# Performance work log

Hardware: AMD Instinct MI355X
Metric: run time of the kernel (lower is better)

## Reference

```python
import jax, jax.numpy as jnp
import numpy as np

B, C, H, W = 16, 1536, 32, 32
M = 64      # num_clusters
L = 128     # cluster_dim
G = 256     # token_dim
HID = 512
OT_ITERS = 3
EPS = 1e-6


def setup_inputs() -> dict:
    key = jax.random.key(0)
    ks = jax.random.split(key, 12)
    def w(k, shape, fan_in):
        return jax.random.normal(k, shape, jnp.float32) * (1.0 / np.sqrt(fan_in))
    return {
        'x': jax.random.normal(ks[0], (B, C, H, W), jnp.float32),
        't': jax.random.normal(ks[1], (B, C), jnp.float32),
        # token_features: Linear(C->512), ReLU, Linear(512->G)
        'Wt1': w(ks[2], (HID, C), C), 'bt1': jnp.zeros((HID,), jnp.float32),
        'Wt2': w(ks[3], (G, HID), HID), 'bt2': jnp.zeros((G,), jnp.float32),
        # cluster_features: 1x1 Conv(C->512), ReLU, 1x1 Conv(512->L)
        'Wc1': w(ks[4], (HID, C), C), 'bc1': jnp.zeros((HID,), jnp.float32),
        'Wc2': w(ks[5], (L, HID), HID), 'bc2': jnp.zeros((L,), jnp.float32),
        # score: 1x1 Conv(C->512), ReLU, 1x1 Conv(512->M)
        'Ws1': w(ks[6], (HID, C), C), 'bs1': jnp.zeros((HID,), jnp.float32),
        'Ws2': w(ks[7], (M, HID), HID), 'bs2': jnp.zeros((M,), jnp.float32),
        # temp_predictor: Conv1d(L->1, k=1)
        'Wtp': w(ks[8], (L,), L), 'btp': jnp.zeros((), jnp.float32),
        'dust_bin': jnp.asarray(1.0, jnp.float32),
        'burst_b': jnp.asarray(0.0, jnp.float32),
        'burst_p': jnp.asarray(1.0, jnp.float32),
        'lambda_discount': jnp.asarray(0.5, jnp.float32),
    }


def _log_optimal_transport(scores, alpha, iters):
    # scores: [B, m, n]; alpha: scalar dust-bin logit
    b, m, n = scores.shape
    Z0 = jnp.concatenate([scores, jnp.broadcast_to(alpha, (b, 1, n))], axis=1)  # [B, m+1, n]
    norm = -jnp.log(jnp.asarray(m + n, scores.dtype))
    log_mu = jnp.concatenate([jnp.full((m,), norm, scores.dtype),
                              (jnp.log(jnp.asarray(n, scores.dtype)) + norm)[None]])  # [m+1]
    log_nu = jnp.full((n,), norm, scores.dtype)
    u = jnp.zeros((b, m + 1), scores.dtype)
    v = jnp.zeros((b, n), scores.dtype)
    for _ in range(iters):
        u = log_mu - jax.nn.logsumexp(Z0 + v[:, None, :], axis=2)
        v = log_nu - jax.nn.logsumexp(Z0 + u[:, :, None], axis=1)
    return Z0 + u[:, :, None] + v[:, None, :] - norm


def _l2norm(a, axis):
    return a / jnp.maximum(jnp.linalg.norm(a, axis=axis, keepdims=True), 1e-12)


def _forward(x, t, Wt1, bt1, Wt2, bt2, Wc1, bc1, Wc2, bc2, Ws1, bs1, Ws2, bs2,
             Wtp, btp, dust_bin, burst_b, burst_p, lambda_discount):
    b, c, h, w = x.shape
    n = h * w
    xf = x.reshape(b, c, n)  # [B, C, N] (1x1 convs == per-pixel MLP)
    # cluster features f: [B, L, N]
    h1 = jax.nn.relu(jnp.einsum('bcn,oc->bon', xf, Wc1) + bc1[:, None])
    f = jnp.einsum('bhn,lh->bln', h1, Wc2) + bc2[:, None]
    # assignment scores p: [B, M, N]
    h2 = jax.nn.relu(jnp.einsum('bcn,oc->bon', xf, Ws1) + bs1[:, None])
    p = jnp.einsum('bhn,mh->bmn', h2, Ws2) + bs2[:, None]
    # global token: [B, G]
    tok = jax.nn.relu(t @ Wt1.T + bt1) @ Wt2.T + bt2
    # Sinkhorn OT soft assignment, drop dust bin row
    P = jnp.exp(_log_optimal_transport(p, dust_bin, OT_ITERS))[:, :-1, :]  # [B, M, N]
    # burst-aware weighting
    f_norm = _l2norm(f, axis=1)                                  # [B, L, N]
    T_i = jax.nn.softplus(jnp.einsum('bln,l->bn', f, Wtp) + btp)  # [B, N]
    sim = jnp.einsum('bli,blj->bij', f_norm, f_norm)              # [B, N, N]
    T_avg = (T_i[:, :, None] + T_i[:, None, :]) * 0.5
    burst_w = jax.nn.sigmoid(T_avg * sim + burst_b)
    discount = jnp.clip(jnp.sum(burst_w, axis=-1) ** burst_p, 1e-3, 1e3)  # [B, N]
    lam = jax.nn.sigmoid(lambda_discount)
    P_adj = (1.0 - lam) * P + lam * (P / (discount[:, None, :] + EPS))
    # local aggregation: (f[:, :, None, :] * P[:, None, :, :]).sum(-1) == batched matmul
    agg = jnp.einsum('bln,bmn->blm', f, P_adj)  # [B, L, M]
    agg = _l2norm(agg, axis=1).reshape(b, -1)   # [B, L*M]
    tok_n = _l2norm(tok, axis=-1)
    g = jnp.concatenate([tok_n, agg], axis=-1)  # [B, G + L*M]
    return _l2norm(g, axis=-1)


def reference(x, t, Wt1, bt1, Wt2, bt2, Wc1, bc1, Wc2, bc2, Ws1, bs1, Ws2, bs2,
              Wtp, btp, dust_bin, burst_b, burst_p, lambda_discount):
    return _forward(x, t, Wt1, bt1, Wt2, bt2, Wc1, bc1, Wc2, bc2, Ws1, bs1, Ws2, bs2,
                    Wtp, btp, dust_bin, burst_b, burst_p, lambda_discount)
```

## Files before the change

kernel.cpp:

```cpp
#include <hip/hip_runtime.h>
#include <math.h>

#define B_   16
#define C_   1536
#define N_   1024
#define M_   64
#define L_   128
#define G_   256
#define HID_ 512

typedef __attribute__((ext_vector_type(8))) short short8;
typedef __attribute__((ext_vector_type(4))) float floatx4;

__device__ __forceinline__ unsigned short f2bf_rne(float x) {
    unsigned u = __float_as_uint(x);
    unsigned r = u + 0x7fffu + ((u >> 16) & 1u);
    return (unsigned short)(r >> 16);
}
__device__ __forceinline__ unsigned pack_bf2(float lo, float hi) {
    unsigned a = __float_as_uint(lo) + 0x8000u;
    unsigned b = __float_as_uint(hi) + 0x8000u;
    return (a >> 16) | (b & 0xffff0000u);
}

__device__ __forceinline__ void gl2lds16(const void* g, void* l) {
    __builtin_amdgcn_global_load_lds(
        (const __attribute__((address_space(1))) void*)g,
        (__attribute__((address_space(3))) void*)l, 16, 0, 0);
}

__global__ __launch_bounds__(256) void cast_w_kernel(
    const float* __restrict__ Wc1, const float* __restrict__ Ws1,
    const float* __restrict__ Wc2, const float* __restrict__ Ws2,
    unsigned short* __restrict__ Wbf, unsigned short* __restrict__ W2)
{
    const int V1 = 393216;
    const int VH = 196608;
    int idx = blockIdx.x * 256 + threadIdx.x;
    if (idx < V1) {
        const float4* src = (idx < VH) ? (const float4*)Wc1 : (const float4*)Ws1;
        float4 v = src[(idx < VH) ? idx : idx - VH];
        ushort4 o;
        o.x = f2bf_rne(v.x); o.y = f2bf_rne(v.y);
        o.z = f2bf_rne(v.z); o.w = f2bf_rne(v.w);
        ((ushort4*)Wbf)[idx] = o;
    } else if (idx < V1 + 192 * 1024) {
        int i2 = idx - V1;
        int row = i2 >> 10, k = i2 & 1023;
        float v = 0.f;
        if (row < 128) { if (k < 512) v = Wc2[row * 512 + k]; }
        else           { if (k >= 512) v = Ws2[(row - 128) * 512 + (k - 512)]; }
        W2[i2] = f2bf_rne(v);
    }
}

__global__ __launch_bounds__(256) void xt_kernel(
    const float* __restrict__ x, unsigned short* __restrict__ xT)
{
    __shared__ float Xs[64][65];
    const int t = threadIdx.x;
    const int n0 = blockIdx.x * 64, c0 = blockIdx.y * 64, b = blockIdx.z;
    const float* xb = x + (long)b * C_ * N_;
    #pragma unroll
    for (int it = 0; it < 16; ++it) {
        int idx = it * 256 + t, cr = idx >> 6, nc = idx & 63;
        Xs[cr][nc] = xb[(long)(c0 + cr) * N_ + n0 + nc];
    }
    __syncthreads();
    unsigned* xo = (unsigned*)(xT + (long)b * N_ * C_);
    #pragma unroll
    for (int it = 0; it < 8; ++it) {
        int idx = it * 256 + t, nr = idx >> 5, pc = idx & 31;
        xo[(long)(n0 + nr) * 768 + (c0 >> 1) + pc] =
            pack_bf2(Xs[2 * pc][nr], Xs[2 * pc + 1][nr]);
    }
}

#define G1_STAGE_A(kt, q)                                                    \
    gl2lds16(aSrc + (long)(q) * (32 * C_) + (kt) * 64,                       \
             (char*)g1lds + (((kt) & 1) * 65536 + (q) * 8192) + sdst)
#define G1_STAGE_B(kt, q)                                                    \
    gl2lds16(bSrc + (long)(q) * (32 * C_) + (kt) * 64,                       \
             (char*)g1lds + (((kt) & 1) * 65536 + 32768 + (q) * 8192) + sdst)

#define G1_PHASE(q, STAGES, TAIL)                                            \
  {                                                                          \
    const char* ab = cb + aFB + (q) * 8192;                                  \
    short8 a0 = *(const short8*)(ab + ks0);                                  \
    short8 a1 = *(const short8*)(ab + ks1);                                  \
    short8 a2 = *(const short8*)(ab + 2048 + ks0);                           \
    short8 a3 = *(const short8*)(ab + 2048 + ks1);                           \
    STAGES                                                                   \
    __builtin_amdgcn_s_barrier();                                            \
    asm volatile("s_waitcnt lgkmcnt(0)" ::: "memory");                       \
    __builtin_amdgcn_sched_barrier(0);                                       \
    __builtin_amdgcn_s_setprio(1);                                           \
    _Pragma("unroll")                                                        \
    for (int fj = 0; fj < 4; ++fj) {                                         \
      acc[2*(q)][fj]   = __builtin_amdgcn_mfma_f32_16x16x32_bf16(            \
          a0, bfr[fj][0], acc[2*(q)][fj], 0, 0, 0);                          \
      acc[2*(q)][fj]   = __builtin_amdgcn_mfma_f32_16x16x32_bf16(            \
          a1, bfr[fj][1], acc[2*(q)][fj], 0, 0, 0);                          \
      acc[2*(q)+1][fj] = __builtin_amdgcn_mfma_f32_16x16x32_bf16(            \
          a2, bfr[fj][0], acc[2*(q)+1][fj], 0, 0, 0);                        \
      acc[2*(q)+1][fj] = __builtin_amdgcn_mfma_f32_16x16x32_bf16(            \
          a3, bfr[fj][1], acc[2*(q)+1][fj], 0, 0, 0);                        \
    }                                                                        \
    __builtin_amdgcn_s_setprio(0);                                           \
    TAIL                                                                     \
    __builtin_amdgcn_s_barrier();                                            \
    __builtin_amdgcn_sched_barrier(0);                                       \
  }

#define G1_TILE(tt, S1, S2, TAIL3)                                           \
  {                                                                          \
    const char* cb = (const char*)g1lds + ((tt) & 1) * 65536;                \
    _Pragma("unroll")                                                        \
    for (int fj = 0; fj < 4; ++fj) {                                         \
      const char* bb = cb + bFB + (fj >> 1) * 8192 + (fj & 1) * 2048;        \
      bfr[fj][0] = *(const short8*)(bb + ks0);                               \
      bfr[fj][1] = *(const short8*)(bb + ks1);                               \
    }                                                                        \
    G1_PHASE(0, if (S1) { G1_STAGE_A((tt)+1, 2); G1_STAGE_A((tt)+1, 3); }, ) \
    G1_PHASE(1, if (S2) { G1_STAGE_B((tt)+2, 0); G1_STAGE_B((tt)+2, 1); }, ) \
    G1_PHASE(2, if (S2) { G1_STAGE_B((tt)+2, 2); G1_STAGE_B((tt)+2, 3); }, ) \
    G1_PHASE(3, if (S2) { G1_STAGE_A((tt)+2, 0); G1_STAGE_A((tt)+2, 1); }, TAIL3) \
  }

__global__ __launch_bounds__(512, 2) void gemm1_kernel(
    const unsigned short* __restrict__ Wbf, const unsigned short* __restrict__ xT,
    const float* __restrict__ bc1, const float* __restrict__ bs1,
    unsigned short* __restrict__ hT)
{
    __shared__ unsigned short g1lds[65536];
    const int t = threadIdx.x;
    const int lane = t & 63, w = t >> 6;
    const int n0 = blockIdx.x * 256, o0 = blockIdx.y * 256, b = blockIdx.z;

    const int sgrow = ((t & 256) ? 128 : 0) + ((t >> 3) & 31);
    const int sdst  = t * 16;
    const int sslot = ((t & 7) ^ ((t >> 3) & 7)) * 8;
    const unsigned short* aSrc = Wbf + (long)(o0 + sgrow) * C_ + sslot;
    const unsigned short* bSrc = xT + (long)b * N_ * C_
                               + (long)(n0 + sgrow) * C_ + sslot;

    const int lrow = lane & 15, kgrp = lane >> 4;
    const int wo = (w >> 2) * 128, wn = (w & 3) * 64;
    const int aFB = (w >> 2) * 4096 + lrow * 128;
    const int bFB = 32768 + ((w >> 1) & 1) * 4096 + (w & 1) * 16384 + lrow * 128;
    const int ks0 = (kgrp ^ (lrow & 7)) * 16;
    const int ks1 = ((4 + kgrp) ^ (lrow & 7)) * 16;

    floatx4 acc[8][4];
    #pragma unroll
    for (int i = 0; i < 8; ++i)
        #pragma unroll
        for (int j = 0; j < 4; ++j) acc[i][j] = (floatx4)0.0f;
    short8 bfr[4][2];

    #pragma unroll
    for (int q = 0; q < 4; ++q) { G1_STAGE_A(0, q); G1_STAGE_B(0, q); }
    #pragma unroll
    for (int q = 0; q < 4; ++q) G1_STAGE_B(1, q);
    G1_STAGE_A(1, 0); G1_STAGE_A(1, 1);
    asm volatile("s_waitcnt vmcnt(6)" ::: "memory");
    __builtin_amdgcn_s_barrier();
    __builtin_amdgcn_sched_barrier(0);

    #pragma unroll 2
    for (int t8 = 0; t8 < 22; ++t8)
        G1_TILE(t8, 1, 1, asm volatile("s_waitcnt vmcnt(6)" ::: "memory");)
    G1_TILE(22, 1, 0, asm volatile("s_waitcnt vmcnt(0)" ::: "memory");)
    G1_TILE(23, 0, 0, )

    const float* bias = (o0 < 512) ? bc1 : bs1;
    const int ob = (o0 < 512) ? o0 : o0 - 512;
    #pragma unroll
    for (int fi = 0; fi < 8; ++fi) {
        const int orow = wo + fi * 16 + kgrp * 4;
        float4 bv = *(const float4*)&bias[ob + orow];
        #pragma unroll
        for (int fj = 0; fj < 4; ++fj) {
            const int n = n0 + wn + fj * 16 + lrow;
            float v0 = fmaxf(acc[fi][fj][0] + bv.x, 0.f);
            float v1 = fmaxf(acc[fi][fj][1] + bv.y, 0.f);
            float v2 = fmaxf(acc[fi][fj][2] + bv.z, 0.f);
            float v3 = fmaxf(acc[fi][fj][3] + bv.w, 0.f);
            uint2 pk;
            pk.x = ((unsigned)f2bf_rne(v0)) | (((unsigned)f2bf_rne(v1)) << 16);
            pk.y = ((unsigned)f2bf_rne(v2)) | (((unsigned)f2bf_rne(v3)) << 16);
            *(uint2*)&hT[((long)b * N_ + n) * 1024 + o0 + orow] = pk;
        }
    }
}

__global__ __launch_bounds__(256, 2) void gemm23_kernel(
    const unsigned short* __restrict__ W2, const unsigned short* __restrict__ hT,
    const float* __restrict__ bc2, const float* __restrict__ bs2,
    float* __restrict__ f, float* __restrict__ p)
{
    __shared__ unsigned short As[64 * 32];
    __shared__ unsigned short Bs[128 * 32];
    const int t = threadIdx.x;
    const int lane = t & 63, w = t >> 6;
    const int n0 = blockIdx.x * 128, o0 = blockIdx.y * 64, b = blockIdx.z;
    const unsigned short* hTb = hT + (long)b * N_ * 1024;

    const int wo = (w >> 1) * 32, wn = (w & 1) * 64;
    const int lrow = lane & 15, kgrp = lane >> 4;
    const int arow = t >> 2, acol = (t & 3) * 8;
    const int klo = (o0 < 128) ? 0 : 512;

    floatx4 acc[2][4];
    #pragma unroll
    for (int i = 0; i < 2; ++i)
        #pragma unroll
        for (int j = 0; j < 4; ++j) acc[i][j] = (floatx4)0.0f;

    for (int k0 = 0; k0 < 512; k0 += 32) {
        gl2lds16(W2 + (long)(o0 + arow) * 1024 + klo + k0 + acol, (char*)As + t * 16);
        #pragma unroll
        for (int r = 0; r < 2; ++r)
            gl2lds16(hTb + (long)(n0 + r * 64 + arow) * 1024 + klo + k0 + acol,
                     (char*)Bs + r * 4096 + t * 16);
        __syncthreads();
        short8 af[2], bfr[4];
        #pragma unroll
        for (int i = 0; i < 2; ++i)
            af[i] = *(const short8*)((const char*)As +
                        (wo + i * 16 + lrow) * 64 + kgrp * 16);
        #pragma unroll
        for (int j = 0; j < 4; ++j)
            bfr[j] = *(const short8*)((const char*)Bs +
                        (wn + j * 16 + lrow) * 64 + kgrp * 16);
        #pragma unroll
        for (int i = 0; i < 2; ++i)
            #pragma unroll
            for (int j = 0; j < 4; ++j)
                acc[i][j] = __builtin_amdgcn_mfma_f32_16x16x32_bf16(
                    af[i], bfr[j], acc[i][j], 0, 0, 0);
        __syncthreads();
    }

    #pragma unroll
    for (int i = 0; i < 2; ++i) {
        int o = o0 + wo + i * 16 + kgrp * 4;
        #pragma unroll
        for (int j = 0; j < 4; ++j) {
            int n = n0 + wn + j * 16 + lrow;
            #pragma unroll
            for (int r = 0; r < 4; ++r) {
                int oo = o + r;
                float v = acc[i][j][r];
                if (oo < 128) f[((long)b * L_ + oo) * N_ + n] = v + bc2[oo];
                else p[((long)b * M_ + (oo - 128)) * N_ + n] = v + bs2[oo - 128];
            }
        }
    }
}

__global__ __launch_bounds__(256) void token1_kernel(
    const float* __restrict__ t_in, const float* __restrict__ Wt1,
    const float* __restrict__ bt1, float* __restrict__ hid)
{
    const int lane = threadIdx.x & 63, w = threadIdx.x >> 6;
    const int o = blockIdx.x * 4 + w, b = blockIdx.y;
    const float4* wr = (const float4*)(Wt1 + (long)o * C_);
    const float4* tb = (const float4*)(t_in + (long)b * C_);
    float acc = 0.f;
    #pragma unroll
    for (int i = 0; i < 6; ++i) {
        float4 a = wr[i * 64 + lane], tv = tb[i * 64 + lane];
        acc += a.x * tv.x + a.y * tv.y + a.z * tv.z + a.w * tv.w;
    }
    #pragma unroll
    for (int off = 1; off < 64; off <<= 1) acc += __shfl_xor(acc, off);
    if (lane == 0) hid[b * HID_ + o] = fmaxf(acc + bt1[o], 0.f);
}

__global__ __launch_bounds__(256) void token2_kernel(
    const float* __restrict__ hid, const float* __restrict__ Wt2,
    const float* __restrict__ bt2, float* __restrict__ tok)
{
    const int lane = threadIdx.x & 63, w = threadIdx.x >> 6;
    const int g = blockIdx.x * 4 + w, b = blockIdx.y;
    const float4* wr = (const float4*)(Wt2 + (long)g * HID_);
    const float4* hb = (const float4*)(hid + (long)b * HID_);
    float acc = 0.f;
    #pragma unroll
    for (int i = 0; i < 2; ++i) {
        float4 a = wr[i * 64 + lane], hv = hb[i * 64 + lane];
        acc += a.x * hv.x + a.y * hv.y + a.z * hv.z + a.w * hv.w;
    }
    #pragma unroll
    for (int off = 1; off < 64; off <<= 1) acc += __shfl_xor(acc, off);
    if (lane == 0) tok[b * G_ + g] = acc + bt2[g];
}

__global__ __launch_bounds__(256) void token3_kernel(
    const float* __restrict__ tok, float* __restrict__ tokn)
{
    __shared__ float red[4];
    const int b = blockIdx.x, t = threadIdx.x;
    float v = tok[b * G_ + t];
    float ss = v * v;
    #pragma unroll
    for (int off = 1; off < 64; off <<= 1) ss += __shfl_xor(ss, off);
    if ((t & 63) == 0) red[t >> 6] = ss;
    __syncthreads();
    float inv = 1.f / fmaxf(sqrtf(red[0] + red[1] + red[2] + red[3]), 1e-12f);
    tokn[b * G_ + t] = v * inv;
}

template<bool FIRST>
__global__ __launch_bounds__(256) void ku_kernel(
    float* __restrict__ p, const float* __restrict__ dust,
    const float* __restrict__ bvec, float* __restrict__ avec)
{
    const int t = threadIdx.x, lane = t & 63, w = t >> 6;
    const int m = blockIdx.x * 4 + w, b = blockIdx.y;
    if (m > M_) return;
    const float* bv = bvec + b * N_;
    float s = 0.f;
    if (m < M_) {
        float* row = p + ((long)b * M_ + m) * N_;
        #pragma unroll
        for (int i = 0; i < 16; ++i) {
            int n = i * 64 + lane;
            if (FIRST) {
                float K = expf(row[n]);
                row[n] = K;
                s += K;
            } else {
                s += row[n] * bv[n];
            }
        }
    } else {
        float ea = expf(dust[0]);
        if (FIRST) s = 16.f * ea;
        else {
            #pragma unroll
            for (int i = 0; i < 16; ++i) s += bv[i * 64 + lane];
            s *= ea;
        }
    }
    #pragma unroll
    for (int off = 1; off < 64; off <<= 1) s += __shfl_xor(s, off);
    if (lane == 0) {
        float mu = (m < M_) ? (1.f / 1088.f) : (1024.f / 1088.f);
        avec[b * (M_ + 1) + m] = mu / s;
    }
}

__global__ __launch_bounds__(256) void kv_kernel(
    const float* __restrict__ K, const float* __restrict__ dust,
    const float* __restrict__ avec, float* __restrict__ bvec)
{
    __shared__ float a_s[M_ + 1];
    const int t = threadIdx.x, b = blockIdx.y;
    const int n = blockIdx.x * 256 + t;
    if (t < M_ + 1) a_s[t] = avec[b * (M_ + 1) + t];
    __syncthreads();
    float s = expf(dust[0]) * a_s[M_];
    const float* col = K + (long)b * M_ * N_ + n;
    #pragma unroll
    for (int m = 0; m < M_; ++m) s = fmaf(col[(long)m * N_], a_s[m], s);
    bvec[b * N_ + n] = (1.f / 1088.f) / s;
}

__global__ __launch_bounds__(256) void tnorm_kernel(
    const float* __restrict__ f, const float* __restrict__ Wtp,
    const float* __restrict__ btp, unsigned short* __restrict__ fnT,
    float* __restrict__ T, float* __restrict__ draw, float* __restrict__ aggz)
{
    __shared__ float Ft[L_][65];
    __shared__ float red_ss[4][64];
    __shared__ float red_dot[4][64];
    __shared__ float invs[64];
    __shared__ float wtp_s[L_];
    const int b = blockIdx.y, n0 = blockIdx.x * 64, t = threadIdx.x;
    const float* fb = f + (long)b * L_ * N_;

    if (t < L_) wtp_s[t] = Wtp[t];
    for (int it = 0; it < 32; ++it) {
        int idx = it * 256 + t;
        int l = idx >> 6, c = idx & 63;
        Ft[l][c] = fb[(long)l * N_ + n0 + c];
    }
    __syncthreads();
    {
        const int lg = t >> 6, col = t & 63;
        float ss = 0.f, dot = 0.f;
        #pragma unroll
        for (int i = 0; i < 32; ++i) {
            int l = lg * 32 + i;
            float v = Ft[l][col];
            ss = fmaf(v, v, ss);
            dot = fmaf(v, wtp_s[l], dot);
        }
        red_ss[lg][col] = ss;
        red_dot[lg][col] = dot;
    }
    {
        int base = (b * 16 + blockIdx.x) * 512;
        aggz[base + t] = 0.f;
        aggz[base + 256 + t] = 0.f;
    }
    __syncthreads();
    if (t < 64) {
        float ss = ((red_ss[0][t] + red_ss[1][t]) + (red_ss[2][t] + red_ss[3][t]));
        float dot = ((red_dot[0][t] + red_dot[1][t]) + (red_dot[2][t] + red_dot[3][t]));
        invs[t] = 1.f / fmaxf(sqrtf(ss), 1e-12f);
        float xx = dot + btp[0];
        T[b * N_ + n0 + t] = (xx > 0.f) ? (xx + log1pf(expf(-xx)))
                                        : log1pf(expf(xx));
        draw[b * N_ + n0 + t] = 0.f;
    }
    __syncthreads();
    unsigned* fo = (unsigned*)fnT;
    for (int it = 0; it < 16; ++it) {
        int idx = it * 256 + t;
        int nl = idx >> 6, jp = idx & 63;
        float inv = invs[nl];
        fo[(((long)b * N_ + n0 + nl) << 6) + jp] =
            pack_bf2(Ft[2 * jp][nl] * inv, Ft[2 * jp + 1][nl] * inv);
    }
}

__global__ __launch_bounds__(256) void sim_kernel(
    const unsigned short* __restrict__ fnT, const float* __restrict__ T,
    const float* __restrict__ bb, float* __restrict__ draw)
{
    __shared__ unsigned short As[64 * 136];
    __shared__ unsigned short Bs[64 * 136];
    __shared__ float Ti[64], Tj[64];
    const int b = blockIdx.z, i0 = blockIdx.y * 64, j0base = blockIdx.x * 256;
    const int t = threadIdx.x, lane = t & 63, w = t >> 6;
    const int lrow = lane & 15, kgrp = lane >> 4;
    const unsigned short* fb = fnT + (long)b * N_ * 128;
    const float burstb = bb[0];

    if (t < 64) Ti[t] = T[b * N_ + i0 + t];
    const int srow = t >> 4, scol = (t & 15) * 8;
    #pragma unroll
    for (int r = 0; r < 4; ++r) {
        uint4 av = *(const uint4*)(fb + (long)(i0 + r * 16 + srow) * 128 + scol);
        *(uint4*)((char*)As + (r * 16 + srow) * 272 + scol * 2) = av;
    }
    uint4 bv[4];
    #pragma unroll
    for (int r = 0; r < 4; ++r)
        bv[r] = *(const uint4*)(fb + (long)(j0base + r * 16 + srow) * 128 + scol);

    float rs[4] = {0.f, 0.f, 0.f, 0.f};
    #pragma unroll
    for (int jj = 0; jj < 4; ++jj) {
        __syncthreads();
        #pragma unroll
        for (int r = 0; r < 4; ++r)
            *(uint4*)((char*)Bs + (r * 16 + srow) * 272 + scol * 2) = bv[r];
        if (t >= 64 && t < 128) Tj[t - 64] = T[b * N_ + j0base + jj * 64 + (t - 64)];
        if (jj < 3) {
            #pragma unroll
            for (int r = 0; r < 4; ++r)
                bv[r] = *(const uint4*)(fb +
                    (long)(j0base + (jj + 1) * 64 + r * 16 + srow) * 128 + scol);
        }
        __syncthreads();

        floatx4 acc[4];
        #pragma unroll
        for (int j = 0; j < 4; ++j) acc[j] = (floatx4)0.0f;
        __builtin_amdgcn_s_setprio(1);
        #pragma unroll
        for (int k0 = 0; k0 < 128; k0 += 32) {
            short8 af = *(const short8*)((const char*)As +
                            (w * 16 + lrow) * 272 + k0 * 2 + kgrp * 16);
            #pragma unroll
            for (int j = 0; j < 4; ++j) {
                short8 bf = *(const short8*)((const char*)Bs +
                                (j * 16 + lrow) * 272 + k0 * 2 + kgrp * 16);
                acc[j] = __builtin_amdgcn_mfma_f32_16x16x32_bf16(af, bf, acc[j], 0, 0, 0);
            }
        }
        __builtin_amdgcn_s_setprio(0);
        #pragma unroll
        for (int j = 0; j < 4; ++j) {
            float Tjv = Tj[j * 16 + lrow];
            #pragma unroll
            for (int r = 0; r < 4; ++r) {
                float Tiv = Ti[w * 16 + kgrp * 4 + r];
                float xarg = 0.5f * (Tiv + Tjv) * acc[j][r] + burstb;
                rs[r] += 1.f / (1.f + expf(-xarg));
            }
        }
    }

    #pragma unroll
    for (int off = 1; off < 16; off <<= 1)
        #pragma unroll
        for (int r = 0; r < 4; ++r) rs[r] += __shfl_xor(rs[r], off);
    if (lrow == 0) {
        #pragma unroll
        for (int r = 0; r < 4; ++r)
            atomicAdd(&draw[b * N_ + i0 + w * 16 + kgrp * 4 + r], rs[r]);
    }
}

__global__ __launch_bounds__(256) void agg_kernel(
    const float* __restrict__ f, const float* __restrict__ Kmat,
    const float* __restrict__ avec, const float* __restrict__ dust,
    const float* __restrict__ draw, const float* __restrict__ bp,
    const float* __restrict__ lamd, float* __restrict__ agg)
{
    __shared__ float fch[L_][65];
    __shared__ float Pch[M_][65];
    __shared__ float a_s[M_ + 1], cf[64];
    const int b = blockIdx.y, n0 = blockIdx.x * 64;
    const int t = threadIdx.x, tx = t & 15, ty = t >> 4;
    const float* fb = f + (long)b * L_ * N_;
    const float* Kb = Kmat + (long)b * M_ * N_;

    if (t < M_ + 1) a_s[t] = avec[b * (M_ + 1) + t];
    __syncthreads();

    for (int idx = t; idx < L_ * 64; idx += 256) {
        int l = idx >> 6, c = idx & 63;
        fch[l][c] = fb[(long)l * N_ + n0 + c];
    }
    for (int idx = t; idx < M_ * 64; idx += 256) {
        int m = idx >> 6, c = idx & 63;
        Pch[m][c] = Kb[(long)m * N_ + n0 + c] * a_s[m];
    }
    __syncthreads();

    if (t < 64) {
        float s = expf(dust[0]) * a_s[M_];
        #pragma unroll
        for (int m = 0; m < M_; ++m) s += Pch[m][t];
        float d = powf(draw[b * N_ + n0 + t], bp[0]);
        d = fminf(fmaxf(d, 1e-3f), 1e3f);
        float lam = 1.f / (1.f + expf(-lamd[0]));
        cf[t] = ((1.f - lam) + lam / (d + 1e-6f)) / s;
    }
    __syncthreads();

    float acc[8][4] = {};
    for (int n = 0; n < 64; ++n) {
        float cfn = cf[n];
        float fv[8], pv[4];
        #pragma unroll
        for (int i = 0; i < 8; ++i) fv[i] = fch[ty + 16 * i][n];
        #pragma unroll
        for (int j = 0; j < 4; ++j) pv[j] = Pch[tx * 4 + j][n] * cfn;
        #pragma unroll
        for (int i = 0; i < 8; ++i)
            #pragma unroll
            for (int j = 0; j < 4; ++j)
                acc[i][j] = fmaf(fv[i], pv[j], acc[i][j]);
    }
    #pragma unroll
    for (int i = 0; i < 8; ++i)
        #pragma unroll
        for (int j = 0; j < 4; ++j)
            atomicAdd(&agg[((long)b * L_ + (ty + 16 * i)) * M_ + tx * 4 + j],
                      acc[i][j]);
}

__global__ __launch_bounds__(256) void final_kernel(
    const float* __restrict__ tokn, const float* __restrict__ agg,
    float* __restrict__ out)
{
    __shared__ float invm[M_];
    __shared__ float red[4];
    __shared__ float s_invtot;
    const int b = blockIdx.x, t = threadIdx.x;
    const float* ab = agg + (long)b * L_ * M_;

    if (t < 64) {
        float ss = 0.f;
        for (int l = 0; l < L_; ++l) {
            float v = ab[l * M_ + t];
            ss = fmaf(v, v, ss);
        }
        invm[t] = 1.f / fmaxf(sqrtf(ss), 1e-12f);
    }
    __syncthreads();

    float part;
    {
        float tn = tokn[b * G_ + t];
        part = tn * tn;
    }
    for (int idx = t; idx < L_ * M_; idx += 256) {
        float v = ab[idx] * invm[idx & 63];
        part = fmaf(v, v, part);
    }
    for (int off = 32; off; off >>= 1) part += __shfl_down(part, off);
    if ((t & 63) == 0) red[t >> 6] = part;
    __syncthreads();
    if (t == 0)
        s_invtot = 1.f / fmaxf(sqrtf(red[0] + red[1] + red[2] + red[3]), 1e-12f);
    __syncthreads();

    const float invtot = s_invtot;
    float* ob = out + (long)b * (G_ + L_ * M_);
    ob[t] = tokn[b * G_ + t] * invtot;
    for (int idx = t; idx < L_ * M_; idx += 256)
        ob[G_ + idx] = ab[idx] * invm[idx & 63] * invtot;
}

extern "C" void kernel_launch(void* const* d_in, const int* in_sizes, int n_in,
                              void* d_out, int out_size, void* d_ws, size_t ws_size,
                              hipStream_t stream)
{
    const float* x    = (const float*)d_in[0];
    const float* t_in = (const float*)d_in[1];
    const float* Wt1  = (const float*)d_in[2];
    const float* bt1  = (const float*)d_in[3];
    const float* Wt2  = (const float*)d_in[4];
    const float* bt2  = (const float*)d_in[5];
    const float* Wc1  = (const float*)d_in[6];
    const float* bc1  = (const float*)d_in[7];
    const float* Wc2  = (const float*)d_in[8];
    const float* bc2  = (const float*)d_in[9];
    const float* Ws1  = (const float*)d_in[10];
    const float* bs1  = (const float*)d_in[11];
    const float* Ws2  = (const float*)d_in[12];
    const float* bs2  = (const float*)d_in[13];
    const float* Wtp  = (const float*)d_in[14];
    const float* btp  = (const float*)d_in[15];
    const float* dust = (const float*)d_in[16];
    const float* bb   = (const float*)d_in[17];
    const float* bp   = (const float*)d_in[18];
    const float* lamd = (const float*)d_in[19];

    char* wsb = (char*)d_ws;
    unsigned short* xT  = (unsigned short*)wsb;
    float* f    = (float*)(wsb + 0);
    float* p    = (float*)(wsb + 8388608);
    unsigned short* fnT = (unsigned short*)(wsb + 12582912);
    float* hid  = (float*)(wsb + 16777216);
    float* tok  = (float*)(wsb + 16809984);
    float* tokn = (float*)(wsb + 16826368);
    float* T    = (float*)(wsb + 16842752);
    float* draw = (float*)(wsb + 16908288);
    float* agg  = (float*)(wsb + 17039360);
    float* avec = (float*)(wsb + 17563648);
    float* bvec = (float*)(wsb + 17567808);
    unsigned short* hT  = (unsigned short*)(wsb + 50331648);
    unsigned short* Wbf = (unsigned short*)(wsb + 83886080);
    unsigned short* W2  = (unsigned short*)(wsb + 87031808);
    float* out  = (float*)d_out;

    cast_w_kernel<<<2304, 256, 0, stream>>>(Wc1, Ws1, Wc2, Ws2, Wbf, W2);

    xt_kernel   <<<dim3(16, 24, 16), 256, 0, stream>>>(x, xT);
    gemm1_kernel<<<dim3(4, 4, 16), 512, 0, stream>>>(Wbf, xT, bc1, bs1, hT);
    gemm23_kernel<<<dim3(8, 3, 16), 256, 0, stream>>>(W2, hT, bc2, bs2, f, p);

    token1_kernel<<<dim3(128, 16), 256, 0, stream>>>(t_in, Wt1, bt1, hid);
    token2_kernel<<<dim3(64, 16), 256, 0, stream>>>(hid, Wt2, bt2, tok);
    token3_kernel<<<16, 256, 0, stream>>>(tok, tokn);

    ku_kernel<true> <<<dim3(17, 16), 256, 0, stream>>>(p, dust, bvec, avec);
    kv_kernel       <<<dim3(4, 16), 256, 0, stream>>>(p, dust, avec, bvec);
    ku_kernel<false><<<dim3(17, 16), 256, 0, stream>>>(p, dust, bvec, avec);
    kv_kernel       <<<dim3(4, 16), 256, 0, stream>>>(p, dust, avec, bvec);
    ku_kernel<false><<<dim3(17, 16), 256, 0, stream>>>(p, dust, bvec, avec);

    tnorm_kernel<<<dim3(16, 16), 256, 0, stream>>>(f, Wtp, btp, fnT, T, draw, agg);
    sim_kernel  <<<dim3(4, 16, 16), 256, 0, stream>>>(fnT, T, bb, draw);
    agg_kernel  <<<dim3(16, 16), 256, 0, stream>>>(f, p, avec, dust, draw, bp, lamd, agg);
    final_kernel<<<16, 256, 0, stream>>>(tokn, agg, out);
}
```

Measured before the change: 384.1 us.

## Fuse Sinkhorn iterations into one persistent kernel with per-batch grid barriers

Replaces the five separate row/column normalization launches with one persistent kernel of 256 blocks. Each block keeps its four exp'd score rows in LDS, accumulates column sums through atomics, and synchronizes the 16 blocks of each batch with a global-atomic spin barrier. The exp is recomputed in agg_kernel instead of writing K back to memory. This removes launch overhead and repeated global reads of the score matrix. In exchange it relies on all 256 blocks being co-resident for the barrier to avoid deadlock, and the atomic float sums are nondeterministic.

```diff
diff --git a/kernel.cpp b/kernel.cpp
--- a/kernel.cpp
+++ b/kernel.cpp
@@ -29,13 +29,26 @@
         (__attribute__((address_space(3))) void*)l, 16, 0, 0);
 }
 
+__device__ __forceinline__ void bar16(unsigned* c, int gen) {
+    __threadfence();
+    __syncthreads();
+    if (threadIdx.x == 0) {
+        __hip_atomic_fetch_add(&c[gen], 1u, __ATOMIC_ACQ_REL, __HIP_MEMORY_SCOPE_AGENT);
+        while (__hip_atomic_load(&c[gen], __ATOMIC_ACQUIRE, __HIP_MEMORY_SCOPE_AGENT) < 16u)
+            __builtin_amdgcn_s_sleep(1);
+    }
+    __syncthreads();
+}
+
 __global__ __launch_bounds__(256) void cast_w_kernel(
     const float* __restrict__ Wc1, const float* __restrict__ Ws1,
     const float* __restrict__ Wc2, const float* __restrict__ Ws2,
-    unsigned short* __restrict__ Wbf, unsigned short* __restrict__ W2)
+    unsigned short* __restrict__ Wbf, unsigned short* __restrict__ W2,
+    float* __restrict__ colsum, unsigned* __restrict__ ctr)
 {
     const int V1 = 393216;
     const int VH = 196608;
+    const int E2 = V1 + 192 * 1024;
     int idx = blockIdx.x * 256 + threadIdx.x;
     if (idx < V1) {
         const float4* src = (idx < VH) ? (const float4*)Wc1 : (const float4*)Ws1;
@@ -44,13 +57,17 @@
         o.x = f2bf_rne(v.x); o.y = f2bf_rne(v.y);
         o.z = f2bf_rne(v.z); o.w = f2bf_rne(v.w);
         ((ushort4*)Wbf)[idx] = o;
-    } else if (idx < V1 + 192 * 1024) {
+    } else if (idx < E2) {
         int i2 = idx - V1;
         int row = i2 >> 10, k = i2 & 1023;
         float v = 0.f;
         if (row < 128) { if (k < 512) v = Wc2[row * 512 + k]; }
         else           { if (k >= 512) v = Ws2[(row - 128) * 512 + (k - 512)]; }
         W2[i2] = f2bf_rne(v);
+    } else if (idx < E2 + 32768) {
+        colsum[idx - E2] = 0.f;
+    } else if (idx < E2 + 32768 + 128) {
+        ctr[idx - E2 - 32768] = 0u;
     }
 }
 
@@ -312,60 +329,116 @@
     tokn[b * G_ + t] = v * inv;
 }
 
-template<bool FIRST>
-__global__ __launch_bounds__(256) void ku_kernel(
-    float* __restrict__ p, const float* __restrict__ dust,
-    const float* __restrict__ bvec, float* __restrict__ avec)
-{
+#define SK_C1 (1.f/1088.f)
+__global__ __launch_bounds__(256) void sinkhorn_persist(
+    const float* __restrict__ p, const float* __restrict__ dust,
+    float* __restrict__ avec, float* __restrict__ colsum,
+    unsigned* __restrict__ ctr)
+{
+    __shared__ float Klds[4][1024];
+    __shared__ float b_lds[1024];
+    __shared__ float a4[4];
+    __shared__ float red[4];
+    const int s = blockIdx.x, b = blockIdx.y;
     const int t = threadIdx.x, lane = t & 63, w = t >> 6;
-    const int m = blockIdx.x * 4 + w, b = blockIdx.y;
-    if (m > M_) return;
-    const float* bv = bvec + b * N_;
-    float s = 0.f;
-    if (m < M_) {
-        float* row = p + ((long)b * M_ + m) * N_;
-        #pragma unroll
-        for (int i = 0; i < 16; ++i) {
-            int n = i * 64 + lane;
-            if (FIRST) {
-                float K = expf(row[n]);
-                row[n] = K;
-                s += K;
-            } else {
-                s += row[n] * bv[n];
-            }
-        }
-    } else {
-        float ea = expf(dust[0]);
-        if (FIRST) s = 16.f * ea;
-        else {
-            #pragma unroll
-            for (int i = 0; i < 16; ++i) s += bv[i * 64 + lane];
-            s *= ea;
-        }
-    }
-    #pragma unroll
-    for (int off = 1; off < 64; off <<= 1) s += __shfl_xor(s, off);
-    if (lane == 0) {
-        float mu = (m < M_) ? (1.f / 1088.f) : (1024.f / 1088.f);
-        avec[b * (M_ + 1) + m] = mu / s;
-    }
-}
-
-__global__ __launch_bounds__(256) void kv_kernel(
-    const float* __restrict__ K, const float* __restrict__ dust,
-    const float* __restrict__ avec, float* __restrict__ bvec)
-{
-    __shared__ float a_s[M_ + 1];
-    const int t = threadIdx.x, b = blockIdx.y;
-    const int n = blockIdx.x * 256 + t;
-    if (t < M_ + 1) a_s[t] = avec[b * (M_ + 1) + t];
-    __syncthreads();
-    float s = expf(dust[0]) * a_s[M_];
-    const float* col = K + (long)b * M_ * N_ + n;
-    #pragma unroll
-    for (int m = 0; m < M_; ++m) s = fmaf(col[(long)m * N_], a_s[m], s);
-    bvec[b * N_ + n] = (1.f / 1088.f) / s;
+    const float ea = expf(dust[0]);
+    const float* prow = p + ((long)b * M_ + s * 4) * N_;
+    float* cs0 = colsum + b * N_;
+    float* cs1 = colsum + 16 * N_ + b * N_;
+    unsigned* cb = ctr + b * 8;
+
+    #pragma unroll
+    for (int it = 0; it < 16; ++it) {
+        int idx = it * 256 + t, r = idx >> 10, n = idx & 1023;
+        Klds[r][n] = expf(prow[(long)r * N_ + n]);
+    }
+    __syncthreads();
+
+    {
+        float sum = 0.f;
+        #pragma unroll
+        for (int i = 0; i < 16; ++i) sum += Klds[w][i * 64 + lane];
+        #pragma unroll
+        for (int off = 1; off < 64; off <<= 1) sum += __shfl_xor(sum, off);
+        if (lane == 0) a4[w] = SK_C1 / sum;
+    }
+    __syncthreads();
+    {
+        float a0 = a4[0], a1 = a4[1], a2 = a4[2], a3 = a4[3];
+        #pragma unroll
+        for (int k = 0; k < 4; ++k) {
+            int n = k * 256 + t;
+            float v = Klds[0][n] * a0 + Klds[1][n] * a1
+                    + Klds[2][n] * a2 + Klds[3][n] * a3;
+            atomicAdd(&cs0[n], v);
+        }
+    }
+    bar16(cb, 0);
+    float Sb1;
+    {
+        float part = 0.f;
+        #pragma unroll
+        for (int k = 0; k < 4; ++k) {
+            int n = k * 256 + t;
+            float bn = SK_C1 / (cs0[n] + SK_C1);
+            b_lds[n] = bn;
+            part += bn;
+        }
+        #pragma unroll
+        for (int off = 1; off < 64; off <<= 1) part += __shfl_xor(part, off);
+        if (lane == 0) red[w] = part;
+        __syncthreads();
+        Sb1 = (red[0] + red[1]) + (red[2] + red[3]);
+    }
+    {
+        float dot = 0.f;
+        #pragma unroll
+        for (int i = 0; i < 16; ++i)
+            dot = fmaf(Klds[w][i * 64 + lane], b_lds[i * 64 + lane], dot);
+        #pragma unroll
+        for (int off = 1; off < 64; off <<= 1) dot += __shfl_xor(dot, off);
+        if (lane == 0) a4[w] = SK_C1 / dot;
+    }
+    __syncthreads();
+    const float eaA2 = (1024.f / 1088.f) / Sb1;
+    {
+        float a0 = a4[0], a1 = a4[1], a2 = a4[2], a3 = a4[3];
+        #pragma unroll
+        for (int k = 0; k < 4; ++k) {
+            int n = k * 256 + t;
+            float v = Klds[0][n] * a0 + Klds[1][n] * a1
+                    + Klds[2][n] * a2 + Klds[3][n] * a3;
+            atomicAdd(&cs1[n], v);
+        }
+    }
+    bar16(cb, 1);
+    float Sb2;
+    {
+        float part = 0.f;
+        #pragma unroll
+        for (int k = 0; k < 4; ++k) {
+            int n = k * 256 + t;
+            float bn = SK_C1 / (cs1[n] + eaA2);
+            b_lds[n] = bn;
+            part += bn;
+        }
+        #pragma unroll
+        for (int off = 1; off < 64; off <<= 1) part += __shfl_xor(part, off);
+        if (lane == 0) red[w] = part;
+        __syncthreads();
+        Sb2 = (red[0] + red[1]) + (red[2] + red[3]);
+    }
+    {
+        float dot = 0.f;
+        #pragma unroll
+        for (int i = 0; i < 16; ++i)
+            dot = fmaf(Klds[w][i * 64 + lane], b_lds[i * 64 + lane], dot);
+        #pragma unroll
+        for (int off = 1; off < 64; off <<= 1) dot += __shfl_xor(dot, off);
+        if (lane == 0) avec[b * (M_ + 1) + s * 4 + w] = SK_C1 / dot;
+    }
+    if (s == 0 && t == 0)
+        avec[b * (M_ + 1) + M_] = (1024.f / 1088.f) / (ea * Sb2);
 }
 
 __global__ __launch_bounds__(256) void tnorm_kernel(
@@ -508,7 +581,7 @@
 }
 
 __global__ __launch_bounds__(256) void agg_kernel(
-    const float* __restrict__ f, const float* __restrict__ Kmat,
+    const float* __restrict__ f, const float* __restrict__ pmat,
     const float* __restrict__ avec, const float* __restrict__ dust,
     const float* __restrict__ draw, const float* __restrict__ bp,
     const float* __restrict__ lamd, float* __restrict__ agg)
@@ -519,7 +592,7 @@
     const int b = blockIdx.y, n0 = blockIdx.x * 64;
     const int t = threadIdx.x, tx = t & 15, ty = t >> 4;
     const float* fb = f + (long)b * L_ * N_;
-    const float* Kb = Kmat + (long)b * M_ * N_;
+    const float* pb = pmat + (long)b * M_ * N_;
 
     if (t < M_ + 1) a_s[t] = avec[b * (M_ + 1) + t];
     __syncthreads();
@@ -530,7 +603,7 @@
     }
     for (int idx = t; idx < M_ * 64; idx += 256) {
         int m = idx >> 6, c = idx & 63;
-        Pch[m][c] = Kb[(long)m * N_ + n0 + c] * a_s[m];
+        Pch[m][c] = expf(pb[(long)m * N_ + n0 + c]) * a_s[m];
     }
     __syncthreads();
 
@@ -647,13 +720,15 @@
     float* draw = (float*)(wsb + 16908288);
     float* agg  = (float*)(wsb + 17039360);
     float* avec = (float*)(wsb + 17563648);
-    float* bvec = (float*)(wsb + 17567808);
     unsigned short* hT  = (unsigned short*)(wsb + 50331648);
     unsigned short* Wbf = (unsigned short*)(wsb + 83886080);
     unsigned short* W2  = (unsigned short*)(wsb + 87031808);
+    float* colsum = (float*)(wsb + 87425024);
+    unsigned* ctr = (unsigned*)(wsb + 87556096);
     float* out  = (float*)d_out;
 
-    cast_w_kernel<<<2304, 256, 0, stream>>>(Wc1, Ws1, Wc2, Ws2, Wbf, W2);
+    cast_w_kernel<<<2433, 256, 0, stream>>>(Wc1, Ws1, Wc2, Ws2, Wbf, W2,
+                                            colsum, ctr);
 
     xt_kernel   <<<dim3(16, 24, 16), 256, 0, stream>>>(x, xT);
     gemm1_kernel<<<dim3(4, 4, 16), 512, 0, stream>>>(Wbf, xT, bc1, bs1, hT);
@@ -663,11 +738,7 @@
     token2_kernel<<<dim3(64, 16), 256, 0, stream>>>(hid, Wt2, bt2, tok);
     token3_kernel<<<16, 256, 0, stream>>>(tok, tokn);
 
-    ku_kernel<true> <<<dim3(17, 16), 256, 0, stream>>>(p, dust, bvec, avec);
-    kv_kernel       <<<dim3(4, 16), 256, 0, stream>>>(p, dust, avec, bvec);
-    ku_kernel<false><<<dim3(17, 16), 256, 0, stream>>>(p, dust, bvec, avec);
-    kv_kernel       <<<dim3(4, 16), 256, 0, stream>>>(p, dust, avec, bvec);
-    ku_kernel<false><<<dim3(17, 16), 256, 0, stream>>>(p, dust, bvec, avec);
+    sinkhorn_persist<<<dim3(16, 16), 256, 0, stream>>>(p, dust, avec, colsum, ctr);
 
     tnorm_kernel<<<dim3(16, 16), 256, 0, stream>>>(f, Wtp, btp, fnT, T, draw, agg);
     sim_kernel  <<<dim3(4, 16, 16), 256, 0, stream>>>(fnT, T, bb, draw);
```

Result: slower. 409.5 us (+6.6%).

## Fuse Sinkhorn column and row updates; remap gemm1 block order across XCDs

Applied to the files above, without the earlier changes.

The separate kv and ku Sinkhorn kernels are merged into one kernel. Each block recomputes the full column-scaling vector for its batch into LDS, then does the row reduction, which cuts the five OT launches to three. Each of the 17 blocks per batch now redundantly reads the whole 256KB K matrix for the column pass, trading extra L2 traffic for fewer launches. Separately, gemm1 block indices are permuted so consecutive hardware-dispatched blocks (round-robined across XCDs) land on the same batch and tiles, to improve L2 locality.

```diff
diff --git a/kernel.cpp b/kernel.cpp
--- a/kernel.cpp
+++ b/kernel.cpp
@@ -135,7 +135,9 @@
     __shared__ unsigned short g1lds[65536];
     const int t = threadIdx.x;
     const int lane = t & 63, w = t >> 6;
-    const int n0 = blockIdx.x * 256, o0 = blockIdx.y * 256, b = blockIdx.z;
+    const int f = blockIdx.x + (blockIdx.y << 2) + (blockIdx.z << 4);
+    const int g = ((f & 7) << 5) + (f >> 3);
+    const int n0 = (g & 3) * 256, o0 = ((g >> 2) & 3) * 256, b = g >> 4;
 
     const int sgrow = ((t & 256) ? 128 : 0) + ((t >> 3) & 31);
     const int sdst  = t * 16;
@@ -312,37 +314,25 @@
     tokn[b * G_ + t] = v * inv;
 }
 
-template<bool FIRST>
-__global__ __launch_bounds__(256) void ku_kernel(
+__global__ __launch_bounds__(256) void ku_first_kernel(
     float* __restrict__ p, const float* __restrict__ dust,
-    const float* __restrict__ bvec, float* __restrict__ avec)
+    float* __restrict__ avec)
 {
     const int t = threadIdx.x, lane = t & 63, w = t >> 6;
     const int m = blockIdx.x * 4 + w, b = blockIdx.y;
     if (m > M_) return;
-    const float* bv = bvec + b * N_;
     float s = 0.f;
     if (m < M_) {
         float* row = p + ((long)b * M_ + m) * N_;
         #pragma unroll
         for (int i = 0; i < 16; ++i) {
             int n = i * 64 + lane;
-            if (FIRST) {
-                float K = expf(row[n]);
-                row[n] = K;
-                s += K;
-            } else {
-                s += row[n] * bv[n];
-            }
+            float K = expf(row[n]);
+            row[n] = K;
+            s += K;
         }
     } else {
-        float ea = expf(dust[0]);
-        if (FIRST) s = 16.f * ea;
-        else {
-            #pragma unroll
-            for (int i = 0; i < 16; ++i) s += bv[i * 64 + lane];
-            s *= ea;
-        }
+        s = 16.f * expf(dust[0]);
     }
     #pragma unroll
     for (int off = 1; off < 64; off <<= 1) s += __shfl_xor(s, off);
@@ -352,20 +342,52 @@
     }
 }
 
-__global__ __launch_bounds__(256) void kv_kernel(
+__global__ __launch_bounds__(256) void kvku_kernel(
     const float* __restrict__ K, const float* __restrict__ dust,
-    const float* __restrict__ avec, float* __restrict__ bvec)
+    const float* __restrict__ avec_in, float* __restrict__ avec_out)
 {
     __shared__ float a_s[M_ + 1];
-    const int t = threadIdx.x, b = blockIdx.y;
-    const int n = blockIdx.x * 256 + t;
-    if (t < M_ + 1) a_s[t] = avec[b * (M_ + 1) + t];
-    __syncthreads();
-    float s = expf(dust[0]) * a_s[M_];
-    const float* col = K + (long)b * M_ * N_ + n;
-    #pragma unroll
-    for (int m = 0; m < M_; ++m) s = fmaf(col[(long)m * N_], a_s[m], s);
-    bvec[b * N_ + n] = (1.f / 1088.f) / s;
+    __shared__ float b_lds[N_];
+    const int t = threadIdx.x, lane = t & 63, w = t >> 6;
+    const int mg = blockIdx.x, b = blockIdx.y;
+    const float ea = expf(dust[0]);
+    const float* Kb = K + (long)b * M_ * N_;
+
+    if (t < M_ + 1) a_s[t] = avec_in[b * (M_ + 1) + t];
+    __syncthreads();
+
+    #pragma unroll
+    for (int k = 0; k < 4; ++k) {
+        int n = k * 256 + t;
+        float s = ea * a_s[M_];
+        const float* col = Kb + n;
+        #pragma unroll
+        for (int m = 0; m < M_; ++m) s = fmaf(col[(long)m * N_], a_s[m], s);
+        b_lds[n] = (1.f / 1088.f) / s;
+    }
+    __syncthreads();
+
+    const int m = mg * 4 + w;
+    if (m > M_) return;
+    float s = 0.f;
+    if (m < M_) {
+        const float* row = Kb + (long)m * N_;
+        #pragma unroll
+        for (int i = 0; i < 16; ++i) {
+            int n = i * 64 + lane;
+            s = fmaf(row[n], b_lds[n], s);
+        }
+    } else {
+        #pragma unroll
+        for (int i = 0; i < 16; ++i) s += b_lds[i * 64 + lane];
+        s *= ea;
+    }
+    #pragma unroll
+    for (int off = 1; off < 64; off <<= 1) s += __shfl_xor(s, off);
+    if (lane == 0) {
+        float mu = (m < M_) ? (1.f / 1088.f) : (1024.f / 1088.f);
+        avec_out[b * (M_ + 1) + m] = mu / s;
+    }
 }
 
 __global__ __launch_bounds__(256) void tnorm_kernel(
@@ -647,7 +669,7 @@
     float* draw = (float*)(wsb + 16908288);
     float* agg  = (float*)(wsb + 17039360);
     float* avec = (float*)(wsb + 17563648);
-    float* bvec = (float*)(wsb + 17567808);
+    float* avec2= (float*)(wsb + 17567808);
     unsigned short* hT  = (unsigned short*)(wsb + 50331648);
     unsigned short* Wbf = (unsigned short*)(wsb + 83886080);
     unsigned short* W2  = (unsigned short*)(wsb + 87031808);
@@ -663,11 +685,9 @@
     token2_kernel<<<dim3(64, 16), 256, 0, stream>>>(hid, Wt2, bt2, tok);
     token3_kernel<<<16, 256, 0, stream>>>(tok, tokn);
 
-    ku_kernel<true> <<<dim3(17, 16), 256, 0, stream>>>(p, dust, bvec, avec);
-    kv_kernel       <<<dim3(4, 16), 256, 0, stream>>>(p, dust, avec, bvec);
-    ku_kernel<false><<<dim3(17, 16), 256, 0, stream>>>(p, dust, bvec, avec);
-    kv_kernel       <<<dim3(4, 16), 256, 0, stream>>>(p, dust, avec, bvec);
-    ku_kernel<false><<<dim3(17, 16), 256, 0, stream>>>(p, dust, bvec, avec);
+    ku_first_kernel<<<dim3(17, 16), 256, 0, stream>>>(p, dust, avec);
+    kvku_kernel    <<<dim3(17, 16), 256, 0, stream>>>(p, dust, avec, avec2);
+    kvku_kernel    <<<dim3(17, 16), 256, 0, stream>>>(p, dust, avec2, avec);
 
     tnorm_kernel<<<dim3(16, 16), 256, 0, stream>>>(f, Wtp, btp, fnT, T, draw, agg);
     sim_kernel  <<<dim3(4, 16, 16), 256, 0, stream>>>(fnT, T, bb, draw);
```

After: 391.9 us. 2.0% more time.
